# Kernel tuning notes

Measured on AMD Instinct MI355X. Metric: run time of the kernel, lower is better.

The kernel has to match this reference:

```python
import jax, jax.numpy as jnp
import numpy as np

HID = 2048
E = 8          # routed experts
TOP_K = 2
F = 1408       # moe_intermediate_size
FS = 2816      # shared expert intermediate
SCALE = 2.5    # routed_scaling_factor


def setup_inputs() -> dict:
    key = jax.random.key(0)
    ks = jax.random.split(key, 8)
    s = 0.02
    return {
        "hidden_states": jax.random.normal(ks[0], (1, 2048, HID), jnp.float32),
        "w_router": jax.random.normal(ks[1], (HID, E), jnp.float32) * s,
        "w_gate": jax.random.normal(ks[2], (E, HID, F), jnp.float32) * s,
        "w_up": jax.random.normal(ks[3], (E, HID, F), jnp.float32) * s,
        "w_down": jax.random.normal(ks[4], (E, F, HID), jnp.float32) * s,
        "ws_gate": jax.random.normal(ks[5], (HID, FS), jnp.float32) * s,
        "ws_up": jax.random.normal(ks[6], (HID, FS), jnp.float32) * s,
        "ws_down": jax.random.normal(ks[7], (FS, HID), jnp.float32) * s,
    }


def reference(hidden_states, w_router, w_gate, w_up, w_down, ws_gate, ws_up, ws_down):
    B, S, D = hidden_states.shape
    x = hidden_states.reshape(-1, D)                      # [T, D]
    T = x.shape[0]

    # --- router: scores = x @ gate.weight.T (w_router is pre-transposed) ---
    probs = jax.nn.softmax(x @ w_router, axis=-1)         # [T, E]
    top_v, top_i = jax.lax.top_k(probs, TOP_K)            # [T, K]
    top_v = top_v / jnp.sum(top_v, axis=-1, keepdims=True)
    # dense combine weights [T, E] (top-k indices are unique per row)
    combine = jnp.zeros((T, E), x.dtype).at[jnp.arange(T)[:, None], top_i].set(top_v)

    # --- routed experts: SwiGLU MLP per expert, masked combine ---
    g = jax.nn.silu(jnp.einsum("td,edf->etf", x, w_gate))
    u = jnp.einsum("td,edf->etf", x, w_up)
    y = jnp.einsum("etf,efd->etd", g * u, w_down)         # [E, T, D]
    routed = jnp.einsum("etd,te->td", y, combine) * SCALE

    # --- shared experts (always-on SwiGLU MLP) ---
    shared = (jax.nn.silu(x @ ws_gate) * (x @ ws_up)) @ ws_down

    return (routed + shared).reshape(B, S, D)
```

## Files before the change

kernel.cpp:

```cpp
#include <hip/hip_runtime.h>
#include <hip/hip_bf16.h>
#include <stdint.h>

#define TOKS 2048
#define DHID 2048
#define NEXP 8
#define FR 1408
#define FS 2816
#define RSCALE 2.5f

#define G1_SH 352
#define G1_GRID 784
#define G1_Q (G1_GRID / 8)
#define G2_SH 256
#define G2_GRID 880
#define G2_Q (G2_GRID / 8)
#define NIMG_WG 2816
#define NIMG_WD 2816
#define NIMG_SG 704
#define NIMG_SD 704
#define WIMG_GRID (NIMG_WG*2 + NIMG_WD + NIMG_SG*2 + NIMG_SD)
#define RW_GRID (512 + WIMG_GRID)

typedef float f32x4 __attribute__((ext_vector_type(4)));
typedef short s16x8 __attribute__((ext_vector_type(8)));

__device__ __forceinline__ ushort f2bf(float f) {
  union { __hip_bfloat16 b; ushort u; } v;
  v.b = __float2bfloat16(f);
  return v.u;
}

__device__ __forceinline__ void gload16(const void* g, void* l) {
  __builtin_amdgcn_global_load_lds(
      (const __attribute__((address_space(1))) unsigned int*)g,
      (__attribute__((address_space(3))) unsigned int*)l, 16, 0, 0);
}

__global__ __launch_bounds__(256) void k_rwimg(
    const float* __restrict__ x, const float* __restrict__ wr,
    ushort* __restrict__ xb, int* __restrict__ top_e, float* __restrict__ top_w,
    const float* __restrict__ wg, const float* __restrict__ wu, const float* __restrict__ wd,
    const float* __restrict__ wsg, const float* __restrict__ wsu, const float* __restrict__ wsd,
    ushort* __restrict__ ig, ushort* __restrict__ iu, ushort* __restrict__ id_,
    ushort* __restrict__ isg, ushort* __restrict__ isu, ushort* __restrict__ isd) {
  if (blockIdx.x < 512) {
    const int wid = threadIdx.x >> 6, lane = threadIdx.x & 63;
    const int t = blockIdx.x * 4 + wid;
    const float* xrow = x + (size_t)t * DHID;
    float acc[NEXP];
#pragma unroll
    for (int e = 0; e < NEXP; ++e) acc[e] = 0.f;
#pragma unroll 4
    for (int j = 0; j < DHID / 64; ++j) {
      const int k = j * 64 + lane;
      const float xv = xrow[k];
      xb[(size_t)t * DHID + k] = f2bf(xv);
      const float4 w0 = *(const float4*)(wr + (size_t)k * 8);
      const float4 w1 = *(const float4*)(wr + (size_t)k * 8 + 4);
      acc[0] += xv * w0.x; acc[1] += xv * w0.y; acc[2] += xv * w0.z; acc[3] += xv * w0.w;
      acc[4] += xv * w1.x; acc[5] += xv * w1.y; acc[6] += xv * w1.z; acc[7] += xv * w1.w;
    }
#pragma unroll
    for (int e = 0; e < NEXP; ++e) {
#pragma unroll
      for (int off = 32; off; off >>= 1) acc[e] += __shfl_xor(acc[e], off);
    }
    if (lane == 0) {
      int i1 = 0;
#pragma unroll
      for (int e = 1; e < NEXP; ++e) if (acc[e] > acc[i1]) i1 = e;
      int i2 = (i1 == 0) ? 1 : 0;
#pragma unroll
      for (int e = 0; e < NEXP; ++e) if (e != i1 && acc[e] > acc[i2]) i2 = e;
      const float w1 = 1.f / (1.f + expf(acc[i2] - acc[i1]));
      top_e[2 * t] = i1; top_e[2 * t + 1] = i2;
      top_w[2 * t] = w1; top_w[2 * t + 1] = 1.f - w1;
    }
    return;
  }
  int id = blockIdx.x - 512;
  const float* src; ushort* dst; int N, ntT, ktT;
  if (id < NIMG_WG)                   { src = wg;  dst = ig;  N = FR;   ntT = 11; ktT = 32; }
  else if ((id -= NIMG_WG) < NIMG_WG) { src = wu;  dst = iu;  N = FR;   ntT = 11; ktT = 32; }
  else if ((id -= NIMG_WG) < NIMG_WD) { src = wd;  dst = id_; N = DHID; ntT = 16; ktT = 22; }
  else if ((id -= NIMG_WD) < NIMG_SG) { src = wsg; dst = isg; N = FS;   ntT = 22; ktT = 32; }
  else if ((id -= NIMG_SG) < NIMG_SG) { src = wsu; dst = isu; N = FS;   ntT = 22; ktT = 32; }
  else { id -= NIMG_SG;                 src = wsd; dst = isd; N = DHID; ntT = 16; ktT = 44; }
  const int per_e = ntT * ktT;
  const int e = id / per_e, rem = id % per_e;
  const int nt = rem / ktT, kt = rem % ktT;
  const int K = ktT * 64;
  src += (size_t)e * K * N;
  dst += (size_t)id * 8192;

  __shared__ float lds[64][133];
  const int tid = threadIdx.x;
#pragma unroll
  for (int j = 0; j < 8; ++j) {
    const int idx = j * 256 + tid;
    const int row = idx >> 5, c4 = (idx & 31) << 2;
    const float4 v = *(const float4*)(src + (size_t)(kt * 64 + row) * N + nt * 128 + c4);
    lds[row][c4] = v.x; lds[row][c4 + 1] = v.y; lds[row][c4 + 2] = v.z; lds[row][c4 + 3] = v.w;
  }
  __syncthreads();
#pragma unroll
  for (int s = 0; s < 4; ++s) {
    const int sid = s * 256 + tid;
    const int col = sid >> 3, ks = sid & 7;
    ushort tmp[8];
#pragma unroll
    for (int j = 0; j < 8; ++j) tmp[j] = f2bf(lds[ks * 8 + j][col]);
    *(s16x8*)((char*)dst + col * 128 + ((ks ^ (col & 7)) * 16)) = *(const s16x8*)&tmp[0];
  }
}

__global__ __launch_bounds__(256) void k_lists(
    const int* __restrict__ top_e, const float* __restrict__ top_w,
    int* __restrict__ offs, int* __restrict__ ptok, float* __restrict__ pw,
    int* __restrict__ meta, int* __restrict__ mtl) {
  __shared__ int cnt[NEXP], fill[NEXP], loff[NEXP + 1];
  const int tid = threadIdx.x;
  if (tid < NEXP) { cnt[tid] = 0; fill[tid] = 0; }
  __syncthreads();
  for (int p = tid; p < 2 * TOKS; p += 256) atomicAdd(&cnt[top_e[p]], 1);
  __syncthreads();
  if (tid == 0) {
    loff[0] = 0;
    for (int e = 0; e < NEXP; ++e) loff[e + 1] = loff[e] + cnt[e];
    int n = 0;
    for (int e = 0; e < NEXP; ++e)
      for (int m = 0; m * 128 < cnt[e]; ++m) mtl[n++] = (e << 8) | m;
    meta[0] = n;
  }
  __syncthreads();
  for (int p = tid; p < 2 * TOKS; p += 256) {
    const int e = top_e[p];
    const int pos = loff[e] + atomicAdd(&fill[e], 1);
    ptok[pos] = p >> 1;
    pw[pos] = top_w[p];
  }
  if (tid < NEXP + 1) offs[tid] = loff[tid];
}

__global__ __launch_bounds__(256, 2) void k_gemm1i(
    const ushort* __restrict__ xb,
    const ushort* __restrict__ ig, const ushort* __restrict__ iu, ushort* __restrict__ Hr,
    const ushort* __restrict__ isg, const ushort* __restrict__ isu, ushort* __restrict__ Hs,
    const int* __restrict__ offs, const int* __restrict__ ptok,
    const int* __restrict__ meta, const int* __restrict__ mtl) {
  constexpr int KT = DHID / 64;
  const int swz = (blockIdx.x & 7) * G1_Q + (blockIdx.x >> 3);
  int mt, nt, N, base, count;
  const char *imgG, *imgU;
  ushort* H;
  bool gather;
  if (swz < G1_SH) {
    mt = swz & 15; nt = swz >> 4;
    base = 0; count = TOKS; N = FS;
    imgG = (const char*)isg + (size_t)(nt * 32) * 16384;
    imgU = (const char*)isu + (size_t)(nt * 32) * 16384;
    H = Hs; gather = false;
  } else {
    const int r = swz - G1_SH;
    const int n_mt = meta[0];
    if (r >= n_mt * 11) return;
    const int tile = mtl[r / 11];
    nt = r % 11;
    const int e = tile >> 8; mt = tile & 255;
    base = offs[e]; count = offs[e + 1] - base; N = FR;
    imgG = (const char*)ig + (size_t)((e * 11 + nt) * 32) * 16384;
    imgU = (const char*)iu + (size_t)((e * 11 + nt) * 32) * 16384;
    H = Hr; gather = true;
  }

  __shared__ char smem[81920];
  const int tid = threadIdx.x, lane = tid & 63, wid = tid >> 6;
  const int wm = wid >> 1, wn = wid & 1;

  const int aj = tid & 7;
  const ushort* aptr[4];
  uint32_t alds[4];
#pragma unroll
  for (int i = 0; i < 4; ++i) {
    const int row = i * 32 + (tid >> 3);
    const int gr = mt * 128 + row;
    const int arow = gather ? ptok[base + (gr < count ? gr : count - 1)] : gr;
    aptr[i] = xb + (size_t)arow * DHID + aj * 8;
    alds[i] = (uint32_t)(row * 128 + ((aj ^ (row & 7)) * 16));
  }

  const f32x4 fz = {0.f, 0.f, 0.f, 0.f};
  f32x4 accg[4][4], accu[4][4];
#pragma unroll
  for (int mi = 0; mi < 4; ++mi)
#pragma unroll
    for (int ni = 0; ni < 4; ++ni) { accg[mi][ni] = fz; accu[mi][ni] = fz; }

  s16x8 areg[4];
#pragma unroll
  for (int i = 0; i < 4; ++i) areg[i] = *(const s16x8*)(aptr[i]);
#pragma unroll
  for (int i = 0; i < 4; ++i) {
    const int o = (i * 4 + wid) * 1024 + lane * 16;
    gload16(imgG + o, smem + 16384 + o);
    gload16(imgU + o, smem + 32768 + o);
  }

  for (int t = 0; t < KT; ++t) {
    const int bufo = 16384 + (t & 1) * 32768;
#pragma unroll
    for (int i = 0; i < 4; ++i) *(s16x8*)(smem + alds[i]) = areg[i];
    __builtin_amdgcn_sched_barrier(0);
    if (t + 1 < KT) {
#pragma unroll
      for (int i = 0; i < 4; ++i) areg[i] = *(const s16x8*)(aptr[i] + (t + 1) * 64);
      const int nbufo = 16384 + ((t + 1) & 1) * 32768;
      const char* gG = imgG + (size_t)(t + 1) * 16384;
      const char* gU = imgU + (size_t)(t + 1) * 16384;
#pragma unroll
      for (int i = 0; i < 4; ++i) {
        const int o = (i * 4 + wid) * 1024 + lane * 16;
        gload16(gG + o, smem + nbufo + o);
        gload16(gU + o, smem + nbufo + 16384 + o);
      }
      asm volatile("s_waitcnt vmcnt(12) lgkmcnt(0)" ::: "memory");
    } else {
      asm volatile("s_waitcnt vmcnt(0) lgkmcnt(0)" ::: "memory");
    }
    __builtin_amdgcn_sched_barrier(0);
    __builtin_amdgcn_s_barrier();
    __builtin_amdgcn_sched_barrier(0);
    __builtin_amdgcn_s_setprio(1);
#pragma unroll
    for (int kk = 0; kk < 64; kk += 32) {
      s16x8 af[4];
#pragma unroll
      for (int mi = 0; mi < 4; ++mi) {
        const int row = wm * 64 + mi * 16 + (lane & 15);
        const int slot = (kk >> 3) + (lane >> 4);
        af[mi] = *(const s16x8*)(smem + row * 128 + ((slot ^ (row & 7)) * 16));
      }
#pragma unroll
      for (int ni = 0; ni < 4; ++ni) {
        const int colg = wn * 64 + ni * 16 + (lane & 15);
        const int slot = (kk >> 3) + (lane >> 4);
        const uint32_t boff = (uint32_t)(colg * 128 + ((slot ^ (colg & 7)) * 16));
        const s16x8 bg = *(const s16x8*)(smem + bufo + boff);
        const s16x8 bu = *(const s16x8*)(smem + bufo + 16384 + boff);
#pragma unroll
        for (int mi = 0; mi < 4; ++mi) {
          accg[mi][ni] = __builtin_amdgcn_mfma_f32_16x16x32_bf16(af[mi], bg, accg[mi][ni], 0, 0, 0);
          accu[mi][ni] = __builtin_amdgcn_mfma_f32_16x16x32_bf16(af[mi], bu, accu[mi][ni], 0, 0, 0);
        }
      }
    }
    __builtin_amdgcn_s_setprio(0);
    __builtin_amdgcn_s_barrier();
  }

#pragma unroll
  for (int mi = 0; mi < 4; ++mi) {
    const int gr0 = mt * 128 + wm * 64 + mi * 16 + ((lane >> 4) << 2);
#pragma unroll
    for (int ni = 0; ni < 4; ++ni) {
      const int nc = nt * 128 + wn * 64 + ni * 16 + (lane & 15);
#pragma unroll
      for (int r = 0; r < 4; ++r) {
        const int gr = gr0 + r;
        if (gr < count) {
          const float g = accg[mi][ni][r];
          const float u = accu[mi][ni][r];
          const float h = g / (1.f + __expf(-g)) * u;
          H[(size_t)(base + gr) * N + nc] = f2bf(h);
        }
      }
    }
  }
}

__global__ __launch_bounds__(256, 2) void k_gemm2i(
    const ushort* __restrict__ Hr, const ushort* __restrict__ id_,
    const ushort* __restrict__ Hs, const ushort* __restrict__ isd,
    float* __restrict__ out, const int* __restrict__ offs,
    const int* __restrict__ ptok, const float* __restrict__ pw,
    const int* __restrict__ meta, const int* __restrict__ mtl) {
  const int swz = (blockIdx.x & 7) * G2_Q + (blockIdx.x >> 3);
  int mt, nt, base, count, K, KT;
  const ushort* Hbuf;
  const char* img;
  bool routed;
  if (swz < G2_SH) {
    mt = swz & 15; nt = swz >> 4;
    base = 0; count = TOKS; K = FS; KT = 44;
    Hbuf = Hs; img = (const char*)isd + (size_t)(nt * 44) * 16384;
    routed = false;
  } else {
    const int r = swz - G2_SH;
    const int n_mt = meta[0];
    if (r >= n_mt * 16) return;
    const int tile = mtl[r / 16];
    nt = r % 16;
    const int e = tile >> 8; mt = tile & 255;
    base = offs[e]; count = offs[e + 1] - base; K = FR; KT = 22;
    Hbuf = Hr; img = (const char*)id_ + (size_t)((e * 16 + nt) * 22) * 16384;
    routed = true;
  }

  __shared__ char smem[49152];
  const int tid = threadIdx.x, lane = tid & 63, wid = tid >> 6;
  const int wm = wid >> 1, wn = wid & 1;

  const int aj = tid & 7;
  const ushort* aptr[4];
  uint32_t alds[4];
#pragma unroll
  for (int i = 0; i < 4; ++i) {
    const int row = i * 32 + (tid >> 3);
    const int gr = mt * 128 + row;
    const int ar = base + (gr < count ? gr : count - 1);
    aptr[i] = Hbuf + (size_t)ar * K + aj * 8;
    alds[i] = (uint32_t)(row * 128 + ((aj ^ (row & 7)) * 16));
  }

  const f32x4 fz = {0.f, 0.f, 0.f, 0.f};
  f32x4 acc[4][4];
#pragma unroll
  for (int mi = 0; mi < 4; ++mi)
#pragma unroll
    for (int ni = 0; ni < 4; ++ni) acc[mi][ni] = fz;

  s16x8 areg[4];
#pragma unroll
  for (int i = 0; i < 4; ++i) areg[i] = *(const s16x8*)(aptr[i]);
#pragma unroll
  for (int i = 0; i < 4; ++i) {
    const int o = (i * 4 + wid) * 1024 + lane * 16;
    gload16(img + o, smem + 16384 + o);
  }

  for (int t = 0; t < KT; ++t) {
    const int bufo = 16384 + (t & 1) * 16384;
#pragma unroll
    for (int i = 0; i < 4; ++i) *(s16x8*)(smem + alds[i]) = areg[i];
    __builtin_amdgcn_sched_barrier(0);
    if (t + 1 < KT) {
#pragma unroll
      for (int i = 0; i < 4; ++i) areg[i] = *(const s16x8*)(aptr[i] + (t + 1) * 64);
      const int nbufo = 16384 + ((t + 1) & 1) * 16384;
      const char* gB = img + (size_t)(t + 1) * 16384;
#pragma unroll
      for (int i = 0; i < 4; ++i) {
        const int o = (i * 4 + wid) * 1024 + lane * 16;
        gload16(gB + o, smem + nbufo + o);
      }
      asm volatile("s_waitcnt vmcnt(8) lgkmcnt(0)" ::: "memory");
    } else {
      asm volatile("s_waitcnt vmcnt(0) lgkmcnt(0)" ::: "memory");
    }
    __builtin_amdgcn_sched_barrier(0);
    __builtin_amdgcn_s_barrier();
    __builtin_amdgcn_sched_barrier(0);
    __builtin_amdgcn_s_setprio(1);
#pragma unroll
    for (int kk = 0; kk < 64; kk += 32) {
      s16x8 af[4];
#pragma unroll
      for (int mi = 0; mi < 4; ++mi) {
        const int row = wm * 64 + mi * 16 + (lane & 15);
        const int slot = (kk >> 3) + (lane >> 4);
        af[mi] = *(const s16x8*)(smem + row * 128 + ((slot ^ (row & 7)) * 16));
      }
#pragma unroll
      for (int ni = 0; ni < 4; ++ni) {
        const int colg = wn * 64 + ni * 16 + (lane & 15);
        const int slot = (kk >> 3) + (lane >> 4);
        const uint32_t boff = (uint32_t)(colg * 128 + ((slot ^ (colg & 7)) * 16));
        const s16x8 bb = *(const s16x8*)(smem + bufo + boff);
#pragma unroll
        for (int mi = 0; mi < 4; ++mi)
          acc[mi][ni] = __builtin_amdgcn_mfma_f32_16x16x32_bf16(af[mi], bb, acc[mi][ni], 0, 0, 0);
      }
    }
    __builtin_amdgcn_s_setprio(0);
    __builtin_amdgcn_s_barrier();
  }

#pragma unroll
  for (int mi = 0; mi < 4; ++mi) {
    const int gr0 = mt * 128 + wm * 64 + mi * 16 + ((lane >> 4) << 2);
#pragma unroll
    for (int ni = 0; ni < 4; ++ni) {
      const int nc = nt * 128 + wn * 64 + ni * 16 + (lane & 15);
#pragma unroll
      for (int r = 0; r < 4; ++r) {
        const int gr = gr0 + r;
        if (gr < count) {
          const int arow = base + gr;
          const float s = routed ? (RSCALE * pw[arow]) : 1.f;
          const int tok = routed ? ptok[arow] : gr;
          unsafeAtomicAdd(out + (size_t)tok * DHID + nc, acc[mi][ni][r] * s);
        }
      }
    }
  }
}

extern "C" void kernel_launch(void* const* d_in, const int* in_sizes, int n_in,
                              void* d_out, int out_size, void* d_ws, size_t ws_size,
                              hipStream_t stream) {
  const float* x   = (const float*)d_in[0];
  const float* wr  = (const float*)d_in[1];
  const float* wg  = (const float*)d_in[2];
  const float* wu  = (const float*)d_in[3];
  const float* wd  = (const float*)d_in[4];
  const float* wsg = (const float*)d_in[5];
  const float* wsu = (const float*)d_in[6];
  const float* wsd = (const float*)d_in[7];
  float* out = (float*)d_out;

  uint8_t* p = (uint8_t*)d_ws;
  ushort* xb   = (ushort*)p; p += (size_t)TOKS * DHID * 2;
  int* top_e   = (int*)p;    p += (size_t)2 * TOKS * 4;
  float* top_w = (float*)p;  p += (size_t)2 * TOKS * 4;
  int* offs    = (int*)p;    p += 256;
  int* meta    = (int*)p;    p += 64;
  int* mtl     = (int*)p;    p += 256;
  int* ptok    = (int*)p;    p += (size_t)2 * TOKS * 4;
  float* pw    = (float*)p;  p += (size_t)2 * TOKS * 4;
  ushort* Hr   = (ushort*)p; p += (size_t)2 * TOKS * FR * 2;
  ushort* Hs   = (ushort*)p; p += (size_t)TOKS * FS * 2;
  ushort* ig   = (ushort*)p; p += (size_t)NIMG_WG * 8192 * 2;
  ushort* iu   = (ushort*)p; p += (size_t)NIMG_WG * 8192 * 2;
  ushort* id_  = (ushort*)p; p += (size_t)NIMG_WD * 8192 * 2;
  ushort* isg  = (ushort*)p; p += (size_t)NIMG_SG * 8192 * 2;
  ushort* isu  = (ushort*)p; p += (size_t)NIMG_SG * 8192 * 2;
  ushort* isd  = (ushort*)p; p += (size_t)NIMG_SD * 8192 * 2;

  hipMemsetAsync(d_out, 0, (size_t)out_size * sizeof(float), stream);
  k_rwimg<<<RW_GRID, 256, 0, stream>>>(x, wr, xb, top_e, top_w,
                                       wg, wu, wd, wsg, wsu, wsd,
                                       ig, iu, id_, isg, isu, isd);
  k_lists<<<1, 256, 0, stream>>>(top_e, top_w, offs, ptok, pw, meta, mtl);
  k_gemm1i<<<G1_GRID, 256, 0, stream>>>(xb, ig, iu, Hr, isg, isu, Hs,
                                        offs, ptok, meta, mtl);
  k_gemm2i<<<G2_GRID, 256, 0, stream>>>(Hr, id_, Hs, isd, out,
                                        offs, ptok, pw, meta, mtl);
}
```

Baseline: 383.6 us.

## Split gate/up GEMM into two sequential K-passes to cut LDS and raise occupancy

```diff
diff --git a/kernel.cpp b/kernel.cpp
--- a/kernel.cpp
+++ b/kernel.cpp
@@ -143,7 +143,7 @@
   if (tid < NEXP + 1) offs[tid] = loff[tid];
 }
 
-__global__ __launch_bounds__(256, 2) void k_gemm1i(
+__global__ __launch_bounds__(256, 3) void k_gemm1i(
     const ushort* __restrict__ xb,
     const ushort* __restrict__ ig, const ushort* __restrict__ iu, ushort* __restrict__ Hr,
     const ushort* __restrict__ isg, const ushort* __restrict__ isu, ushort* __restrict__ Hs,
@@ -174,7 +174,7 @@
     H = Hr; gather = true;
   }
 
-  __shared__ char smem[81920];
+  __shared__ char smem[49152];
   const int tid = threadIdx.x, lane = tid & 63, wid = tid >> 6;
   const int wm = wid >> 1, wn = wid & 1;
 
@@ -198,33 +198,30 @@
     for (int ni = 0; ni < 4; ++ni) { accg[mi][ni] = fz; accu[mi][ni] = fz; }
 
   s16x8 areg[4];
+
 #pragma unroll
   for (int i = 0; i < 4; ++i) areg[i] = *(const s16x8*)(aptr[i]);
 #pragma unroll
   for (int i = 0; i < 4; ++i) {
     const int o = (i * 4 + wid) * 1024 + lane * 16;
     gload16(imgG + o, smem + 16384 + o);
-    gload16(imgU + o, smem + 32768 + o);
-  }
-
+  }
   for (int t = 0; t < KT; ++t) {
-    const int bufo = 16384 + (t & 1) * 32768;
+    const int bufo = 16384 + (t & 1) * 16384;
 #pragma unroll
     for (int i = 0; i < 4; ++i) *(s16x8*)(smem + alds[i]) = areg[i];
     __builtin_amdgcn_sched_barrier(0);
     if (t + 1 < KT) {
 #pragma unroll
       for (int i = 0; i < 4; ++i) areg[i] = *(const s16x8*)(aptr[i] + (t + 1) * 64);
-      const int nbufo = 16384 + ((t + 1) & 1) * 32768;
-      const char* gG = imgG + (size_t)(t + 1) * 16384;
-      const char* gU = imgU + (size_t)(t + 1) * 16384;
+      const int nbufo = 16384 + ((t + 1) & 1) * 16384;
+      const char* gB = imgG + (size_t)(t + 1) * 16384;
 #pragma unroll
       for (int i = 0; i < 4; ++i) {
         const int o = (i * 4 + wid) * 1024 + lane * 16;
-        gload16(gG + o, smem + nbufo + o);
-        gload16(gU + o, smem + nbufo + 16384 + o);
-      }
-      asm volatile("s_waitcnt vmcnt(12) lgkmcnt(0)" ::: "memory");
+        gload16(gB + o, smem + nbufo + o);
+      }
+      asm volatile("s_waitcnt vmcnt(8) lgkmcnt(0)" ::: "memory");
     } else {
       asm volatile("s_waitcnt vmcnt(0) lgkmcnt(0)" ::: "memory");
     }
@@ -247,12 +244,63 @@
         const int slot = (kk >> 3) + (lane >> 4);
         const uint32_t boff = (uint32_t)(colg * 128 + ((slot ^ (colg & 7)) * 16));
         const s16x8 bg = *(const s16x8*)(smem + bufo + boff);
-        const s16x8 bu = *(const s16x8*)(smem + bufo + 16384 + boff);
-#pragma unroll
-        for (int mi = 0; mi < 4; ++mi) {
+#pragma unroll
+        for (int mi = 0; mi < 4; ++mi)
           accg[mi][ni] = __builtin_amdgcn_mfma_f32_16x16x32_bf16(af[mi], bg, accg[mi][ni], 0, 0, 0);
+      }
+    }
+    __builtin_amdgcn_s_setprio(0);
+    __builtin_amdgcn_s_barrier();
+  }
+
+#pragma unroll
+  for (int i = 0; i < 4; ++i) areg[i] = *(const s16x8*)(aptr[i]);
+#pragma unroll
+  for (int i = 0; i < 4; ++i) {
+    const int o = (i * 4 + wid) * 1024 + lane * 16;
+    gload16(imgU + o, smem + 16384 + o);
+  }
+  for (int t = 0; t < KT; ++t) {
+    const int bufo = 16384 + (t & 1) * 16384;
+#pragma unroll
+    for (int i = 0; i < 4; ++i) *(s16x8*)(smem + alds[i]) = areg[i];
+    __builtin_amdgcn_sched_barrier(0);
+    if (t + 1 < KT) {
+#pragma unroll
+      for (int i = 0; i < 4; ++i) areg[i] = *(const s16x8*)(aptr[i] + (t + 1) * 64);
+      const int nbufo = 16384 + ((t + 1) & 1) * 16384;
+      const char* gB = imgU + (size_t)(t + 1) * 16384;
+#pragma unroll
+      for (int i = 0; i < 4; ++i) {
+        const int o = (i * 4 + wid) * 1024 + lane * 16;
+        gload16(gB + o, smem + nbufo + o);
+      }
+      asm volatile("s_waitcnt vmcnt(8) lgkmcnt(0)" ::: "memory");
+    } else {
+      asm volatile("s_waitcnt vmcnt(0) lgkmcnt(0)" ::: "memory");
+    }
+    __builtin_amdgcn_sched_barrier(0);
+    __builtin_amdgcn_s_barrier();
+    __builtin_amdgcn_sched_barrier(0);
+    __builtin_amdgcn_s_setprio(1);
+#pragma unroll
+    for (int kk = 0; kk < 64; kk += 32) {
+      s16x8 af[4];
+#pragma unroll
+      for (int mi = 0; mi < 4; ++mi) {
+        const int row = wm * 64 + mi * 16 + (lane & 15);
+        const int slot = (kk >> 3) + (lane >> 4);
+        af[mi] = *(const s16x8*)(smem + row * 128 + ((slot ^ (row & 7)) * 16));
+      }
+#pragma unroll
+      for (int ni = 0; ni < 4; ++ni) {
+        const int colg = wn * 64 + ni * 16 + (lane & 15);
+        const int slot = (kk >> 3) + (lane >> 4);
+        const uint32_t boff = (uint32_t)(colg * 128 + ((slot ^ (colg & 7)) * 16));
+        const s16x8 bu = *(const s16x8*)(smem + bufo + boff);
+#pragma unroll
+        for (int mi = 0; mi < 4; ++mi)
           accu[mi][ni] = __builtin_amdgcn_mfma_f32_16x16x32_bf16(af[mi], bu, accu[mi][ni], 0, 0, 0);
-        }
       }
     }
     __builtin_amdgcn_s_setprio(0);
```

Result: slower. 417.4 us (+8.8%).

## Move down-projection weight conversion into GEMM1 launch to overlap with compute

Applied to the files above, without the earlier changes.

```diff
diff --git a/kernel.cpp b/kernel.cpp
--- a/kernel.cpp
+++ b/kernel.cpp
@@ -19,8 +19,9 @@
 #define NIMG_WD 2816
 #define NIMG_SG 704
 #define NIMG_SD 704
-#define WIMG_GRID (NIMG_WG*2 + NIMG_WD + NIMG_SG*2 + NIMG_SD)
-#define RW_GRID (512 + WIMG_GRID)
+#define RW_GRID (512 + NIMG_WG * 2 + NIMG_SG * 2)
+#define G1_CONV (NIMG_WD + NIMG_SD)
+#define G1_FULL (G1_GRID + G1_CONV)
 
 typedef float f32x4 __attribute__((ext_vector_type(4)));
 typedef short s16x8 __attribute__((ext_vector_type(8)));
@@ -37,13 +38,38 @@
       (__attribute__((address_space(3))) unsigned int*)l, 16, 0, 0);
 }
 
+__device__ __forceinline__ void conv_panel(
+    const float* __restrict__ src, ushort* __restrict__ dst,
+    int N, int nt, int kt, char* smem) {
+  float (*lds)[133] = (float(*)[133])smem;
+  const int tid = threadIdx.x;
+#pragma unroll
+  for (int j = 0; j < 8; ++j) {
+    const int idx = j * 256 + tid;
+    const int row = idx >> 5, c4 = (idx & 31) << 2;
+    const float4 v = *(const float4*)(src + (size_t)(kt * 64 + row) * N + nt * 128 + c4);
+    lds[row][c4] = v.x; lds[row][c4 + 1] = v.y; lds[row][c4 + 2] = v.z; lds[row][c4 + 3] = v.w;
+  }
+  __syncthreads();
+#pragma unroll
+  for (int s = 0; s < 4; ++s) {
+    const int sid = s * 256 + tid;
+    const int col = sid >> 3, ks = sid & 7;
+    ushort tmp[8];
+#pragma unroll
+    for (int j = 0; j < 8; ++j) tmp[j] = f2bf(lds[ks * 8 + j][col]);
+    *(s16x8*)((char*)dst + col * 128 + ((ks ^ (col & 7)) * 16)) = *(const s16x8*)&tmp[0];
+  }
+}
+
 __global__ __launch_bounds__(256) void k_rwimg(
     const float* __restrict__ x, const float* __restrict__ wr,
     ushort* __restrict__ xb, int* __restrict__ top_e, float* __restrict__ top_w,
-    const float* __restrict__ wg, const float* __restrict__ wu, const float* __restrict__ wd,
-    const float* __restrict__ wsg, const float* __restrict__ wsu, const float* __restrict__ wsd,
-    ushort* __restrict__ ig, ushort* __restrict__ iu, ushort* __restrict__ id_,
-    ushort* __restrict__ isg, ushort* __restrict__ isu, ushort* __restrict__ isd) {
+    const float* __restrict__ wg, const float* __restrict__ wu,
+    const float* __restrict__ wsg, const float* __restrict__ wsu,
+    ushort* __restrict__ ig, ushort* __restrict__ iu,
+    ushort* __restrict__ isg, ushort* __restrict__ isu) {
+  __shared__ char smem[34048];
   if (blockIdx.x < 512) {
     const int wid = threadIdx.x >> 6, lane = threadIdx.x & 63;
     const int t = blockIdx.x * 4 + wid;
@@ -81,38 +107,15 @@
   }
   int id = blockIdx.x - 512;
   const float* src; ushort* dst; int N, ntT, ktT;
-  if (id < NIMG_WG)                   { src = wg;  dst = ig;  N = FR;   ntT = 11; ktT = 32; }
-  else if ((id -= NIMG_WG) < NIMG_WG) { src = wu;  dst = iu;  N = FR;   ntT = 11; ktT = 32; }
-  else if ((id -= NIMG_WG) < NIMG_WD) { src = wd;  dst = id_; N = DHID; ntT = 16; ktT = 22; }
-  else if ((id -= NIMG_WD) < NIMG_SG) { src = wsg; dst = isg; N = FS;   ntT = 22; ktT = 32; }
-  else if ((id -= NIMG_SG) < NIMG_SG) { src = wsu; dst = isu; N = FS;   ntT = 22; ktT = 32; }
-  else { id -= NIMG_SG;                 src = wsd; dst = isd; N = DHID; ntT = 16; ktT = 44; }
+  if (id < NIMG_WG)                   { src = wg;  dst = ig;  N = FR; ntT = 11; ktT = 32; }
+  else if ((id -= NIMG_WG) < NIMG_WG) { src = wu;  dst = iu;  N = FR; ntT = 11; ktT = 32; }
+  else if ((id -= NIMG_WG) < NIMG_SG) { src = wsg; dst = isg; N = FS; ntT = 22; ktT = 32; }
+  else { id -= NIMG_SG;                 src = wsu; dst = isu; N = FS; ntT = 22; ktT = 32; }
   const int per_e = ntT * ktT;
   const int e = id / per_e, rem = id % per_e;
   const int nt = rem / ktT, kt = rem % ktT;
   const int K = ktT * 64;
-  src += (size_t)e * K * N;
-  dst += (size_t)id * 8192;
-
-  __shared__ float lds[64][133];
-  const int tid = threadIdx.x;
-#pragma unroll
-  for (int j = 0; j < 8; ++j) {
-    const int idx = j * 256 + tid;
-    const int row = idx >> 5, c4 = (idx & 31) << 2;
-    const float4 v = *(const float4*)(src + (size_t)(kt * 64 + row) * N + nt * 128 + c4);
-    lds[row][c4] = v.x; lds[row][c4 + 1] = v.y; lds[row][c4 + 2] = v.z; lds[row][c4 + 3] = v.w;
-  }
-  __syncthreads();
-#pragma unroll
-  for (int s = 0; s < 4; ++s) {
-    const int sid = s * 256 + tid;
-    const int col = sid >> 3, ks = sid & 7;
-    ushort tmp[8];
-#pragma unroll
-    for (int j = 0; j < 8; ++j) tmp[j] = f2bf(lds[ks * 8 + j][col]);
-    *(s16x8*)((char*)dst + col * 128 + ((ks ^ (col & 7)) * 16)) = *(const s16x8*)&tmp[0];
-  }
+  conv_panel(src + (size_t)e * K * N, dst + (size_t)id * 8192, N, nt, kt, smem);
 }
 
 __global__ __launch_bounds__(256) void k_lists(
@@ -148,7 +151,22 @@
     const ushort* __restrict__ ig, const ushort* __restrict__ iu, ushort* __restrict__ Hr,
     const ushort* __restrict__ isg, const ushort* __restrict__ isu, ushort* __restrict__ Hs,
     const int* __restrict__ offs, const int* __restrict__ ptok,
-    const int* __restrict__ meta, const int* __restrict__ mtl) {
+    const int* __restrict__ meta, const int* __restrict__ mtl,
+    const float* __restrict__ wd, const float* __restrict__ wsd,
+    ushort* __restrict__ id_, ushort* __restrict__ isd) {
+  __shared__ char smem[81920];
+  if (blockIdx.x >= G1_GRID) {
+    int cid = blockIdx.x - G1_GRID;
+    const float* src; ushort* dst; int ntT, ktT;
+    if (cid < NIMG_WD) { src = wd; dst = id_; ntT = 16; ktT = 22; }
+    else { cid -= NIMG_WD; src = wsd; dst = isd; ntT = 16; ktT = 44; }
+    const int per_e = ntT * ktT;
+    const int e = cid / per_e, rem = cid % per_e;
+    const int nt = rem / ktT, kt = rem % ktT;
+    const int K = ktT * 64;
+    conv_panel(src + (size_t)e * K * DHID, dst + (size_t)cid * 8192, DHID, nt, kt, smem);
+    return;
+  }
   constexpr int KT = DHID / 64;
   const int swz = (blockIdx.x & 7) * G1_Q + (blockIdx.x >> 3);
   int mt, nt, N, base, count;
@@ -174,7 +192,6 @@
     H = Hr; gather = true;
   }
 
-  __shared__ char smem[81920];
   const int tid = threadIdx.x, lane = tid & 63, wid = tid >> 6;
   const int wm = wid >> 1, wn = wid & 1;
 
@@ -439,11 +456,12 @@
 
   hipMemsetAsync(d_out, 0, (size_t)out_size * sizeof(float), stream);
   k_rwimg<<<RW_GRID, 256, 0, stream>>>(x, wr, xb, top_e, top_w,
-                                       wg, wu, wd, wsg, wsu, wsd,
-                                       ig, iu, id_, isg, isu, isd);
+                                       wg, wu, wsg, wsu,
+                                       ig, iu, isg, isu);
   k_lists<<<1, 256, 0, stream>>>(top_e, top_w, offs, ptok, pw, meta, mtl);
-  k_gemm1i<<<G1_GRID, 256, 0, stream>>>(xb, ig, iu, Hr, isg, isu, Hs,
-                                        offs, ptok, meta, mtl);
+  k_gemm1i<<<G1_FULL, 256, 0, stream>>>(xb, ig, iu, Hr, isg, isu, Hs,
+                                        offs, ptok, meta, mtl,
+                                        wd, wsd, id_, isd);
   k_gemm2i<<<G2_GRID, 256, 0, stream>>>(Hr, id_, Hs, isd, out,
                                         offs, ptok, pw, meta, mtl);
 }
```

Result: faster. 361.3 us, median of 13 (-5.8%).
